# Performance work log

Hardware: AMD Instinct MI355X
Metric: run time of the kernel (lower is better)

Reference implementation:

```python
import jax, jax.numpy as jnp
import numpy as np

CH_N = 12
CH_N_CONST = 4
CH_E = 8
MAX_V = 100.0
DT = 1.0


def _build_graph(n_inputs, n_hid, n_actions):
    n_nodes = n_inputs + n_hid + n_actions + 1
    mid = np.arange(n_inputs, n_inputs + n_hid + n_actions)
    src = np.concatenate([
        np.repeat(np.arange(n_inputs), n_hid + n_actions),
        np.repeat(np.arange(n_inputs, n_inputs + n_hid), n_hid + n_actions),
        np.full(n_nodes - 1, n_nodes - 1),
    ])
    tgt = np.concatenate([
        np.tile(mid, n_inputs),
        np.tile(mid, n_hid),
        np.arange(n_nodes - 1),
    ])
    return src.astype(np.int32), tgt.astype(np.int32), n_nodes


def setup_inputs() -> dict:
    n_inputs, n_hid, n_actions, B = 64, 1024, 16, 2
    src, tgt, n_nodes = _build_graph(n_inputs, n_hid, n_actions)
    n_edges = src.shape[0]
    key = jax.random.key(0)
    ks = jax.random.split(key, 10)
    s = 0.05
    d_msg_in = 2 + 2 * CH_N + CH_E          # 34
    d_msg_out = 2 * (CH_N - CH_N_CONST) + CH_E  # 24
    d_upd_in = 3 * CH_N - 2 * CH_N_CONST    # 28
    return {
        "nodes": jax.random.normal(ks[0], (B, n_nodes, CH_N), jnp.float32) * s,
        "edges": jax.random.normal(ks[1], (B, n_edges, CH_E), jnp.float32) * s,
        "msg_w1": jax.random.normal(ks[2], (32, d_msg_in), jnp.float32) * s,
        "msg_b1": jax.random.normal(ks[3], (32,), jnp.float32) * s,
        "msg_w2": jax.random.normal(ks[4], (d_msg_out, 32), jnp.float32) * s,
        "msg_b2": jax.random.normal(ks[5], (d_msg_out,), jnp.float32) * s,
        "upd_w1": jax.random.normal(ks[6], (16, d_upd_in), jnp.float32) * s,
        "upd_b1": jax.random.normal(ks[7], (16,), jnp.float32) * s,
        "upd_w2": jax.random.normal(ks[8], (CH_N - CH_N_CONST, 16), jnp.float32) * s,
        "upd_b2": jax.random.normal(ks[9], (CH_N - CH_N_CONST,), jnp.float32) * s,
        "sources": jnp.asarray(src),
        "targets": jnp.asarray(tgt),
    }


def reference(nodes, edges, msg_w1, msg_b1, msg_w2, msg_b2,
              upd_w1, upd_b1, upd_w2, upd_b2, sources, targets):
    B, N, _ = nodes.shape
    E = edges.shape[1]
    d = CH_N - CH_N_CONST  # dynamic node channels = 8

    # degree features (float for concat)
    out_degs = jax.ops.segment_sum(jnp.ones((E,), nodes.dtype), sources, num_segments=N)
    in_degs = jax.ops.segment_sum(jnp.ones((E,), nodes.dtype), targets, num_segments=N)
    od = jnp.broadcast_to(out_degs[sources][None, :, None], (B, E, 1))
    idg = jnp.broadcast_to(in_degs[targets][None, :, None], (B, E, 1))

    # gather + message MLP: [B, E, 34] -> 32 -> 24
    m_x = jnp.concatenate([nodes[:, sources], nodes[:, targets], edges, od, idg], axis=2)
    h = jax.nn.relu(jnp.einsum('bef,hf->beh', m_x, msg_w1) + msg_b1)
    m = jnp.einsum('beh,oh->beo', h, msg_w2) + msg_b2
    m_a, m_b, m_ab = m[..., :d], m[..., d:2 * d], m[..., 2 * d:]

    # scatter-aggregate (mean)
    agg_a = jnp.zeros((B, N, d), m.dtype).at[:, sources].add(m_a)
    agg_b = jnp.zeros((B, N, d), m.dtype).at[:, targets].add(m_b)
    agg_a = agg_a / jnp.maximum(out_degs, 1.0)[None, :, None]
    agg_b = agg_b / jnp.maximum(in_degs, 1.0)[None, :, None]

    # update MLP: [B, N, 28] -> 16 -> 8
    u_x = jnp.concatenate([agg_a, agg_b, nodes], axis=2)
    uh = jax.nn.relu(jnp.einsum('bnf,hf->bnh', u_x, upd_w1) + upd_b1)
    update = jnp.einsum('bnh,oh->bno', uh, upd_w2) + upd_b2

    # node step (decay=0, set_nodes=False, hard clamp)
    new_dyn = jnp.clip(nodes[..., :d] + update * DT, -MAX_V, MAX_V)
    new_nodes = jnp.concatenate([new_dyn, nodes[..., d:]], axis=-1)
    # edge step (ch_e_const=0, hard clamp)
    new_edges = jnp.clip(edges + m_ab * DT, -MAX_V, MAX_V)
    return new_nodes, new_edges
```

## Files before the change

kernel.cpp:

```cpp
#include <hip/hip_runtime.h>
#include <stdint.h>

#define D_IN1 34
#define H1    32
#define D_IN2 28
#define H2    16
#define CHN   12
#define CHE   8

__device__ __forceinline__ float clip100(float f) { return fminf(fmaxf(f, -100.f), 100.f); }

__global__ void k_zero(int* __restrict__ p, int n_words) {
    int i = blockIdx.x * blockDim.x + threadIdx.x;
    if (i < n_words) p[i] = 0;
}

__global__ void k_degs(const int* __restrict__ src, const int* __restrict__ tgt,
                       int* __restrict__ outd, int* __restrict__ ind, int E, int N) {
    extern __shared__ int hist[];
    int* ho = hist;
    int* hi = hist + N;
    for (int k = threadIdx.x; k < 2 * N; k += blockDim.x) hist[k] = 0;
    __syncthreads();
    for (int e = blockIdx.x * blockDim.x + threadIdx.x; e < E;
         e += gridDim.x * blockDim.x) {
        int s = src[e];
        int t = tgt[e];
        int s0 = __shfl(s, 0);
        unsigned long long act = __ballot(1);
        if (__all(s == s0)) {
            if ((threadIdx.x & 63) == 0) atomicAdd(&ho[s0], (int)__popcll(act));
        } else {
            atomicAdd(&ho[s], 1);
        }
        atomicAdd(&hi[t], 1);
    }
    __syncthreads();
    for (int k = threadIdx.x; k < N; k += blockDim.x) {
        int a = ho[k], b = hi[k];
        if (a) atomicAdd(&outd[k], a);
        if (b) atomicAdd(&ind[k], b);
    }
}

__launch_bounds__(256)
__global__ void k_pre(const float* __restrict__ nodes,
                      const int* __restrict__ outd, const int* __restrict__ ind,
                      const float* __restrict__ w1, const float* __restrict__ b1,
                      float4* __restrict__ SAq, float4* __restrict__ TBq,
                      int N, int Npad, int total) {
    int i = blockIdx.x * blockDim.x + threadIdx.x;
    if (i >= total) return;
    int n = i % N;
    int b = i / N;

    float x[12];
    const float4* np = (const float4*)(nodes + (size_t)i * CHN);
    float4 n0 = np[0], n1 = np[1], n2 = np[2];
    x[0]=n0.x; x[1]=n0.y; x[2]=n0.z; x[3]=n0.w;
    x[4]=n1.x; x[5]=n1.y; x[6]=n1.z; x[7]=n1.w;
    x[8]=n2.x; x[9]=n2.y; x[10]=n2.z; x[11]=n2.w;
    float od  = (float)outd[n];
    float idg = (float)ind[n];

    float sa[H1], tb[H1];
#pragma unroll
    for (int h = 0; h < H1; ++h) {
        const float* wr = w1 + h * D_IN1;
        float a = wr[32] * od;
#pragma unroll
        for (int k = 0; k < 12; ++k) a = fmaf(wr[k], x[k], a);
        sa[h] = a;
        float c = fmaf(wr[33], idg, b1[h]);
#pragma unroll
        for (int k = 0; k < 12; ++k) c = fmaf(wr[12 + k], x[k], c);
        tb[h] = c;
    }
#pragma unroll
    for (int q = 0; q < 8; ++q) {
        size_t idx = (size_t)(b * 8 + q) * Npad + n;
        SAq[idx] = make_float4(sa[4*q], sa[4*q+1], sa[4*q+2], sa[4*q+3]);
        TBq[idx] = make_float4(tb[4*q], tb[4*q+1], tb[4*q+2], tb[4*q+3]);
    }
}

__launch_bounds__(512)
__global__ void k_edge(const float* __restrict__ edges,
                       const float4* __restrict__ SAq, const float4* __restrict__ TBq,
                       const float* __restrict__ w1, const float* __restrict__ w2,
                       const float* __restrict__ b2,
                       const int* __restrict__ src, const int* __restrict__ tgt,
                       float* __restrict__ agg_a, float* __restrict__ partials,
                       float* __restrict__ new_edges, int E, int N, int Npad,
                       int chunk, int nblk_alloc) {
    extern __shared__ float aggB[];
    int blk = blockIdx.x, b = blockIdx.y;
    int start = blk * chunk;
    if (start >= E) return;
    int end = min(E, start + chunk);

    for (int k = threadIdx.x; k < 8 * N; k += 512) aggB[k] = 0.f;
    __syncthreads();

    for (int base = start; base < end; base += 512) {
        int e = base + threadIdx.x;
        bool v = e < end;

        int s = 0, t = 0;
        float ma[8];

        if (v) { s = src[e]; t = tgt[e]; }

        float x[8];
        if (v) {
            const float4* ep = (const float4*)(edges + ((size_t)b * E + e) * CHE);
            float4 p0 = ep[0], p1 = ep[1];
            x[0]=p0.x; x[1]=p0.y; x[2]=p0.z; x[3]=p0.w;
            x[4]=p1.x; x[5]=p1.y; x[6]=p1.z; x[7]=p1.w;
        }

        float4 sa4[8], tb4[8];
#pragma unroll
        for (int q = 0; q < 8; ++q) {
            size_t bq = (size_t)(b * 8 + q) * Npad;
            sa4[q] = SAq[bq + s];
            tb4[q] = TBq[bq + t];
        }

        float h[H1];
#pragma unroll
        for (int q = 0; q < 8; ++q) {
            const float* sp = (const float*)&sa4[q];
            const float* tp = (const float*)&tb4[q];
#pragma unroll
            for (int r = 0; r < 4; ++r) {
                const float* wr = w1 + (4 * q + r) * D_IN1 + 24;
                float a = sp[r] + tp[r];
#pragma unroll
                for (int k = 0; k < 8; ++k) a = fmaf(wr[k], x[k], a);
                h[4 * q + r] = fmaxf(a, 0.f);
            }
        }

        if (v) {
#pragma unroll
            for (int o = 0; o < 8; ++o) {
                float a = b2[16 + o];
#pragma unroll
                for (int j = 0; j < H1; ++j) a = fmaf(w2[(16 + o) * H1 + j], h[j], a);
                x[o] = clip100(x[o] + a);
            }
            float4* ow = (float4*)(new_edges + ((size_t)b * E + e) * CHE);
            ow[0] = make_float4(x[0], x[1], x[2], x[3]);
            ow[1] = make_float4(x[4], x[5], x[6], x[7]);

#pragma unroll
            for (int o = 0; o < 8; ++o) {
                float a = b2[8 + o];
#pragma unroll
                for (int j = 0; j < H1; ++j) a = fmaf(w2[(8 + o) * H1 + j], h[j], a);
                atomicAdd(&aggB[o * N + t], a);
            }

#pragma unroll
            for (int o = 0; o < 8; ++o) {
                float a = b2[o];
#pragma unroll
                for (int j = 0; j < H1; ++j) a = fmaf(w2[o * H1 + j], h[j], a);
                ma[o] = a;
            }
        }

        int s0 = __shfl(s, 0);
        bool fast = __all(v && s == s0);
        if (fast) {
            float* ga = agg_a + ((size_t)b * N + s0) * 8;
#pragma unroll
            for (int c = 0; c < 8; ++c) {
                float vv = ma[c];
#pragma unroll
                for (int off = 32; off; off >>= 1) vv += __shfl_xor(vv, off);
                if ((threadIdx.x & 63) == 0) atomicAdd(&ga[c], vv);
            }
        } else if (v) {
            float* ga = agg_a + ((size_t)b * N + s) * 8;
#pragma unroll
            for (int c = 0; c < 8; ++c) atomicAdd(&ga[c], ma[c]);
        }
    }

    __syncthreads();
    float* P = partials + ((size_t)b * nblk_alloc + blk) * 8 * N;
    for (int k = threadIdx.x; k < 8 * N; k += 512) P[k] = aggB[k];
}

__global__ void k_aggb(const float* __restrict__ partials, float* __restrict__ agg_b,
                       int nblk_used, int nblk_alloc, int span, int N, int totb) {
    int id = blockIdx.x * blockDim.x + threadIdx.x;
    if (id >= totb) return;
    int p0 = blockIdx.y * span;
    int p1 = min(nblk_used, p0 + span);
    if (p0 >= p1) return;
    int b = id / (8 * N);
    int r = id % (8 * N);
    float sum = 0.f;
    for (int p = p0; p < p1; ++p)
        sum += partials[((size_t)b * nblk_alloc + p) * 8 * N + r];
    atomicAdd(&agg_b[(size_t)b * 8 * N + r], sum);
}

__launch_bounds__(256)
__global__ void k_upd(const float* __restrict__ nodes,
                      const float* __restrict__ agg_a, const float* __restrict__ agg_b,
                      const int* __restrict__ outd, const int* __restrict__ ind,
                      const float* __restrict__ u1, const float* __restrict__ ub1,
                      const float* __restrict__ u2, const float* __restrict__ ub2,
                      float* __restrict__ new_nodes, int N, int total) {
    int i = blockIdx.x * blockDim.x + threadIdx.x;
    if (i >= total) return;
    int b = i / N;
    int n = i % N;

    float rod = 1.f / fmaxf((float)outd[n], 1.f);
    float rdg = 1.f / fmaxf((float)ind[n], 1.f);

    float ux[D_IN2];
    const float4* ga = (const float4*)(agg_a + (size_t)i * 8);
    float4 a0 = ga[0], a1 = ga[1];
    ux[0] = a0.x * rod; ux[1] = a0.y * rod; ux[2] = a0.z * rod; ux[3] = a0.w * rod;
    ux[4] = a1.x * rod; ux[5] = a1.y * rod; ux[6] = a1.z * rod; ux[7] = a1.w * rod;
    const float* gb = agg_b + (size_t)b * 8 * N + n;
#pragma unroll
    for (int c = 0; c < 8; ++c) ux[8 + c] = gb[(size_t)c * N] * rdg;

    const float4* np4 = (const float4*)(nodes + (size_t)i * CHN);
    float4 n0 = np4[0], n1 = np4[1], n2 = np4[2];
    ux[16] = n0.x; ux[17] = n0.y; ux[18] = n0.z; ux[19] = n0.w;
    ux[20] = n1.x; ux[21] = n1.y; ux[22] = n1.z; ux[23] = n1.w;
    ux[24] = n2.x; ux[25] = n2.y; ux[26] = n2.z; ux[27] = n2.w;

    float hb[H2];
#pragma unroll
    for (int h = 0; h < H2; ++h) {
        float a = ub1[h];
#pragma unroll
        for (int k = 0; k < D_IN2; ++k) a = fmaf(u1[h * D_IN2 + k], ux[k], a);
        hb[h] = fmaxf(a, 0.f);
    }
#pragma unroll
    for (int o = 0; o < 8; ++o) {
        float a = ub2[o];
#pragma unroll
        for (int k = 0; k < H2; ++k) a = fmaf(u2[o * H2 + k], hb[k], a);
        ux[16 + o] = clip100(ux[16 + o] + a);
    }
    float4* onp = (float4*)(new_nodes + (size_t)i * CHN);
    onp[0] = make_float4(ux[16], ux[17], ux[18], ux[19]);
    onp[1] = make_float4(ux[20], ux[21], ux[22], ux[23]);
    onp[2] = n2;
}

extern "C" void kernel_launch(void* const* d_in, const int* in_sizes, int n_in,
                              void* d_out, int out_size, void* d_ws, size_t ws_size,
                              hipStream_t stream) {
    const float* nodes = (const float*)d_in[0];
    const float* edges = (const float*)d_in[1];
    const float* mw1   = (const float*)d_in[2];
    const float* mb1   = (const float*)d_in[3];
    const float* mw2   = (const float*)d_in[4];
    const float* mb2   = (const float*)d_in[5];
    const float* uw1   = (const float*)d_in[6];
    const float* ubb1  = (const float*)d_in[7];
    const float* uw2   = (const float*)d_in[8];
    const float* ubb2  = (const float*)d_in[9];
    const int* src     = (const int*)d_in[10];
    const int* tgt     = (const int*)d_in[11];

    int E = in_sizes[10];
    int B = in_sizes[1] / (E * 8);
    int N = in_sizes[0] / (B * 12);
    int Npad = (N + 63) & ~63;

    size_t off = 0;
    int* outd = (int*)((char*)d_ws + off);       off += (size_t)N * 4;
    int* ind  = (int*)((char*)d_ws + off);       off += (size_t)N * 4;
    off = (off + 63) & ~(size_t)63;
    float* agg_a = (float*)((char*)d_ws + off);  off += (size_t)B * N * 8 * 4;
    float* agg_b = (float*)((char*)d_ws + off);  off += (size_t)B * N * 8 * 4;
    size_t zbytes = off;
    off = (off + 63) & ~(size_t)63;
    float4* SAq = (float4*)((char*)d_ws + off);  off += (size_t)B * 8 * Npad * 16;
    float4* TBq = (float4*)((char*)d_ws + off);  off += (size_t)B * 8 * Npad * 16;
    off = (off + 63) & ~(size_t)63;
    float* partials = (float*)((char*)d_ws + off);

    size_t per_blk = (size_t)B * 8 * N * sizeof(float);
    size_t avail = (ws_size > off) ? (ws_size - off) : 0;
    int nblk = (int)(avail / per_blk);
    if (nblk > 512) nblk = 512;
    if (nblk < 8)   nblk = 8;

    int zwords = (int)(zbytes / 4);
    k_zero<<<(zwords + 255) / 256, 256, 0, stream>>>((int*)d_ws, zwords);

    k_degs<<<256, 256, 2 * N * sizeof(int), stream>>>(src, tgt, outd, ind, E, N);

    int totn = B * N;
    k_pre<<<(totn + 255) / 256, 256, 0, stream>>>(nodes, outd, ind, mw1, mb1,
                                                  SAq, TBq, N, Npad, totn);

    float* out_nodes = (float*)d_out;
    float* out_edges = out_nodes + (size_t)B * N * 12;

    int chunk = (E + nblk - 1) / nblk;
    chunk = (chunk + 511) & ~511;
    int nblk_used = (E + chunk - 1) / chunk;

    dim3 ge(nblk_used, B);
    k_edge<<<ge, 512, 8 * N * sizeof(float), stream>>>(
        edges, SAq, TBq, mw1, mw2, mb2, src, tgt,
        agg_a, partials, out_edges, E, N, Npad, chunk, nblk);

    int totb = B * 8 * N;
    const int P = 16;
    int span = (nblk_used + P - 1) / P;
    dim3 ga((totb + 255) / 256, P);
    k_aggb<<<ga, 256, 0, stream>>>(partials, agg_b, nblk_used, nblk, span, N, totb);

    k_upd<<<(totn + 255) / 256, 256, 0, stream>>>(nodes, agg_a, agg_b, outd, ind,
                                                  uw1, ubb1, uw2, ubb2,
                                                  out_nodes, N, totn);
}
```

Measured before the change: 380.0 us.

## Prefetch next edge indices, hoist gathers, move agg zeroing into k_pre

Software-pipelines the edge loop by loading the src/tgt indices for the next 512-edge tile during the current iteration, and issues the SA/TB gathers before the edge-feature load so their latency overlaps. The MLP output computations are taken out of the validity branch so they run unconditionally. Zeroing of agg_a/agg_b moves from k_zero into k_pre, which shrinks the zeroing kernel to the degree counters. The cost is extra registers for the prefetched indices and wasted work on inactive lanes, which could reduce occupancy.

```diff
diff --git a/kernel.cpp b/kernel.cpp
--- a/kernel.cpp
+++ b/kernel.cpp
@@ -48,11 +48,18 @@
                       const int* __restrict__ outd, const int* __restrict__ ind,
                       const float* __restrict__ w1, const float* __restrict__ b1,
                       float4* __restrict__ SAq, float4* __restrict__ TBq,
+                      float* __restrict__ agg_a, float* __restrict__ agg_b,
                       int N, int Npad, int total) {
     int i = blockIdx.x * blockDim.x + threadIdx.x;
     if (i >= total) return;
     int n = i % N;
     int b = i / N;
+
+    float4 z4 = make_float4(0.f, 0.f, 0.f, 0.f);
+    float4* ga4 = (float4*)(agg_a + (size_t)i * 8);
+    ga4[0] = z4; ga4[1] = z4;
+#pragma unroll
+    for (int c = 0; c < 8; ++c) agg_b[(size_t)b * 8 * N + (size_t)c * N + n] = 0.f;
 
     float x[12];
     const float4* np = (const float4*)(nodes + (size_t)i * CHN);
@@ -102,14 +109,21 @@
     for (int k = threadIdx.x; k < 8 * N; k += 512) aggB[k] = 0.f;
     __syncthreads();
 
+    int e0i = start + (int)threadIdx.x;
+    int s = 0, t = 0;
+    if (e0i < end) { s = src[e0i]; t = tgt[e0i]; }
+
     for (int base = start; base < end; base += 512) {
-        int e = base + threadIdx.x;
+        int e = base + (int)threadIdx.x;
         bool v = e < end;
 
-        int s = 0, t = 0;
-        float ma[8];
-
-        if (v) { s = src[e]; t = tgt[e]; }
+        float4 sa4[8], tb4[8];
+        size_t bq0 = (size_t)b * 8 * Npad;
+#pragma unroll
+        for (int q = 0; q < 8; ++q) {
+            sa4[q] = SAq[bq0 + (size_t)q * Npad + s];
+            tb4[q] = TBq[bq0 + (size_t)q * Npad + t];
+        }
 
         float x[8];
         if (v) {
@@ -119,13 +133,9 @@
             x[4]=p1.x; x[5]=p1.y; x[6]=p1.z; x[7]=p1.w;
         }
 
-        float4 sa4[8], tb4[8];
-#pragma unroll
-        for (int q = 0; q < 8; ++q) {
-            size_t bq = (size_t)(b * 8 + q) * Npad;
-            sa4[q] = SAq[bq + s];
-            tb4[q] = TBq[bq + t];
-        }
+        int e2 = base + 512 + (int)threadIdx.x;
+        int s2 = 0, t2 = 0;
+        if (e2 < end) { s2 = src[e2]; t2 = tgt[e2]; }
 
         float h[H1];
 #pragma unroll
@@ -142,37 +152,44 @@
             }
         }
 
+#pragma unroll
+        for (int o = 0; o < 8; ++o) {
+            float a = b2[16 + o];
+#pragma unroll
+            for (int j = 0; j < H1; ++j) a = fmaf(w2[(16 + o) * H1 + j], h[j], a);
+            x[o] = clip100(x[o] + a);
+        }
         if (v) {
-#pragma unroll
-            for (int o = 0; o < 8; ++o) {
-                float a = b2[16 + o];
-#pragma unroll
-                for (int j = 0; j < H1; ++j) a = fmaf(w2[(16 + o) * H1 + j], h[j], a);
-                x[o] = clip100(x[o] + a);
-            }
             float4* ow = (float4*)(new_edges + ((size_t)b * E + e) * CHE);
             ow[0] = make_float4(x[0], x[1], x[2], x[3]);
             ow[1] = make_float4(x[4], x[5], x[6], x[7]);
-
-#pragma unroll
-            for (int o = 0; o < 8; ++o) {
-                float a = b2[8 + o];
-#pragma unroll
-                for (int j = 0; j < H1; ++j) a = fmaf(w2[(8 + o) * H1 + j], h[j], a);
-                atomicAdd(&aggB[o * N + t], a);
-            }
-
-#pragma unroll
-            for (int o = 0; o < 8; ++o) {
-                float a = b2[o];
-#pragma unroll
-                for (int j = 0; j < H1; ++j) a = fmaf(w2[o * H1 + j], h[j], a);
-                ma[o] = a;
-            }
-        }
-
-        int s0 = __shfl(s, 0);
-        bool fast = __all(v && s == s0);
+        }
+
+        float ma[8];
+#pragma unroll
+        for (int o = 0; o < 8; ++o) {
+            float a = b2[o];
+#pragma unroll
+            for (int j = 0; j < H1; ++j) a = fmaf(w2[o * H1 + j], h[j], a);
+            ma[o] = a;
+        }
+        float mb[8];
+#pragma unroll
+        for (int o = 0; o < 8; ++o) {
+            float a = b2[8 + o];
+#pragma unroll
+            for (int j = 0; j < H1; ++j) a = fmaf(w2[(8 + o) * H1 + j], h[j], a);
+            mb[o] = a;
+        }
+
+        if (v) {
+#pragma unroll
+            for (int c = 0; c < 8; ++c) atomicAdd(&aggB[c * N + t], mb[c]);
+        }
+
+        int su = v ? s : -1;
+        int s0 = __shfl(su, 0);
+        bool fast = __all(v && su == s0);
         if (fast) {
             float* ga = agg_a + ((size_t)b * N + s0) * 8;
 #pragma unroll
@@ -187,6 +204,8 @@
 #pragma unroll
             for (int c = 0; c < 8; ++c) atomicAdd(&ga[c], ma[c]);
         }
+
+        s = s2; t = t2;
     }
 
     __syncthreads();
@@ -284,10 +303,10 @@
     size_t off = 0;
     int* outd = (int*)((char*)d_ws + off);       off += (size_t)N * 4;
     int* ind  = (int*)((char*)d_ws + off);       off += (size_t)N * 4;
+    size_t zbytes = off;
     off = (off + 63) & ~(size_t)63;
     float* agg_a = (float*)((char*)d_ws + off);  off += (size_t)B * N * 8 * 4;
     float* agg_b = (float*)((char*)d_ws + off);  off += (size_t)B * N * 8 * 4;
-    size_t zbytes = off;
     off = (off + 63) & ~(size_t)63;
     float4* SAq = (float4*)((char*)d_ws + off);  off += (size_t)B * 8 * Npad * 16;
     float4* TBq = (float4*)((char*)d_ws + off);  off += (size_t)B * 8 * Npad * 16;
@@ -307,7 +326,8 @@
 
     int totn = B * N;
     k_pre<<<(totn + 255) / 256, 256, 0, stream>>>(nodes, outd, ind, mw1, mb1,
-                                                  SAq, TBq, N, Npad, totn);
+                                                  SAq, TBq, agg_a, agg_b,
+                                                  N, Npad, totn);
 
     float* out_nodes = (float*)d_out;
     float* out_edges = out_nodes + (size_t)B * N * 12;
```

After: 439.7 us. 1.16x slower.
